# Kernel optimization log

Hardware: AMD Instinct MI355X
Metric: run time of the kernel (lower is better)

The kernel has to match this reference:

```python
import jax, jax.numpy as jnp
import numpy as np

# Coarse-to-fine lossless 3D segmentation (Seg3dLossless), batch=1, C=1.
RES = [17, 33, 65, 129]          # odd resolutions, stride (RF-1)/(R-1) is integral
RF = RES[-1]
B_MIN, B_MAX = -1.0, 1.0
BAL = 0.5                        # balance_value
N_CONFLICT_ITERS = 2             # fixed unroll of the data-dependent while-loop


def _mlp(pts, w1, b1, w2, b2, w3, b3):
    # query_func: occupancy MLP on normalized (x,y,z) points -> [N]
    h = jax.nn.relu(pts @ w1 + b1)
    h = jax.nn.relu(h @ w2 + b2)
    return jax.nn.sigmoid(h @ w3 + b3)[..., 0]


def _eval_grid(R, w1, b1, w2, b2, w3, b3):
    # batch_eval with align_corners=False: coords2D = (coord + 0.5)/RF, mapped to [B_MIN,B_MAX]
    s = (RF - 1) // (R - 1)
    c = jnp.arange(R, dtype=jnp.float32) * s                 # final-res integer coords
    p = (c + 0.5) / RF * (B_MAX - B_MIN) + B_MIN
    zz, yy, xx = jnp.meshgrid(p, p, p, indexing='ij')        # [D,H,W]
    pts = jnp.stack([xx, yy, zz], axis=-1).reshape(-1, 3)    # (x,y,z) order
    return _mlp(pts, w1, b1, w2, b2, w3, b3).reshape(R, R, R)


def _resize(x, R):
    # trilinear, align_corners=True: out index j -> in coord j*(in-1)/(out-1)
    c = jnp.linspace(0.0, x.shape[0] - 1.0, R)
    zz, yy, xx = jnp.meshgrid(c, c, c, indexing='ij')
    return jax.scipy.ndimage.map_coordinates(x, [zz, yy, xx], order=1, mode='nearest')


def _dilate(m):
    # smooth_conv3x3 (mean filter) followed by >0 == 3x3x3 binary dilation
    f = jax.lax.reduce_window(m.astype(jnp.float32), 0.0, jax.lax.max,
                              (3, 3, 3), (1, 1, 1), 'SAME')
    return f > 0.0


def setup_inputs() -> dict:
    key = jax.random.key(0)
    k1, k2, k3 = jax.random.split(key, 3)
    H = 64
    return {
        'w1': jax.random.normal(k1, (3, H), jnp.float32) * 0.8,
        'b1': jnp.zeros((H,), jnp.float32),
        'w2': jax.random.normal(k2, (H, H), jnp.float32) * (1.0 / np.sqrt(H)),
        'b2': jnp.zeros((H,), jnp.float32),
        'w3': jax.random.normal(k3, (H, 1), jnp.float32) * (1.0 / np.sqrt(H)),
        'b3': jnp.zeros((1,), jnp.float32),
    }


def reference(w1, b1, w2, b2, w3, b3):
    params = (w1, b1, w2, b2, w3, b3)
    # level 0: dense eval on the coarse grid
    occ = _eval_grid(RES[0], *params)                        # [R0,R0,R0]
    s0 = (RF - 1) // (RES[0] - 1)
    calculated = jnp.zeros((RF, RF, RF), bool).at[::s0, ::s0, ::s0].set(True)

    for R in RES[1:]:
        s = (RF - 1) // (R - 1)
        valid = _resize((occ > BAL).astype(jnp.float32), R)  # no-grad mask path
        occ_i = _resize(occ, R)                              # differentiable interp
        boundary = _dilate((valid > 0.0) & (valid < 1.0))
        calc_l = calculated[::s, ::s, ::s]
        boundary = boundary & (~calc_l)                      # skip already-evaluated voxels
        occ_true = _eval_grid(R, *params)                    # query_func at this level
        occ = jnp.where(boundary, occ_true, occ_i)           # scatter of occupancys_topk
        calc_l = calc_l | boundary
        # conflict resolution: re-query 3^3 neighbors of sign-flip voxels
        conflict = boundary & ((occ_i - BAL) * (occ_true - BAL) < 0.0)
        for _ in range(N_CONFLICT_ITERS):
            nbr = _dilate(conflict) & (~calc_l)
            occ_prev = occ
            occ = jnp.where(nbr, occ_true, occ)
            calc_l = calc_l | nbr
            conflict = nbr & ((occ_prev - BAL) * (occ_true - BAL) < 0.0)
        calculated = calculated.at[::s, ::s, ::s].set(calc_l)

    return occ[None, None]                                   # (1, 1, D, H, W)
```

## Files before the change

kernel.cpp:

```cpp
#include <hip/hip_runtime.h>

#define HH 64

static __global__ void k_set_ones(unsigned char* __restrict__ p, int n){
  int i = blockIdx.x * blockDim.x + threadIdx.x;
  if (i < n) p[i] = 1;
}

static __global__ void k_prep_w2t(const float* __restrict__ w2, float* __restrict__ w2t){
  int t = blockIdx.x * 256 + threadIdx.x;
  w2t[t] = w2[(t & 63) * HH + (t >> 6)];
}

static __global__ void k_eval_mlp(
    const float* __restrict__ w1, const float* __restrict__ b1,
    const float* __restrict__ w2t, const float* __restrict__ b2,
    const float* __restrict__ w3, const float* __restrict__ b3,
    float* __restrict__ out, int R, int s)
{
  __shared__ float sw1[3*HH];
  __shared__ float sb1[HH];
  __shared__ float sw2t[HH*HH];
  __shared__ float sb2[HH];
  __shared__ float sw3[HH];
  __shared__ float sb3s[1];
  const int t = threadIdx.x;
  {
    const float4* src4 = (const float4*)w2t;
    float4* dst4 = (float4*)sw2t;
    for (int idx = t; idx < HH*HH/4; idx += 256) dst4[idx] = src4[idx];
  }
  if (t < 3*HH) sw1[t] = w1[t];
  if (t < HH){ sb1[t] = b1[t]; sb2[t] = b2[t]; sw3[t] = w3[t]; }
  if (t == 0) sb3s[0] = b3[0];
  __syncthreads();

  const unsigned int n = (unsigned int)R * (unsigned int)R * (unsigned int)R;
  const int lane = t & 63;
  const int half = lane >> 5;
  const int ibase = half * 32;
  const unsigned int gwave = (blockIdx.x * 256u + (unsigned int)t) >> 6;
  const unsigned int pid = gwave * 32u + (unsigned int)(lane & 31);
  if (pid >= n) return;

  const unsigned int c = pid % (unsigned int)R;
  const unsigned int r = pid / (unsigned int)R;
  const unsigned int b = r % (unsigned int)R;
  const unsigned int a = r / (unsigned int)R;
  const float inv129x2 = 2.0f / 129.0f;
  const float x = ((float)(c * (unsigned int)s) + 0.5f) * inv129x2 - 1.0f;
  const float y = ((float)(b * (unsigned int)s) + 0.5f) * inv129x2 - 1.0f;
  const float z = ((float)(a * (unsigned int)s) + 0.5f) * inv129x2 - 1.0f;

  float h1[32];
  #pragma unroll
  for (int k = 0; k < 32; ++k){
    int i = ibase + k;
    float v = sb1[i];
    v = fmaf(x, sw1[i],        v);
    v = fmaf(y, sw1[HH + i],   v);
    v = fmaf(z, sw1[2*HH + i], v);
    h1[k] = fmaxf(v, 0.0f);
  }
  float o = sb3s[0];
  #pragma unroll 4
  for (int j = 0; j < HH; ++j){
    const float* wr = &sw2t[j*HH + ibase];
    float acc = 0.0f;
    #pragma unroll
    for (int k = 0; k < 32; ++k) acc = fmaf(h1[k], wr[k], acc);
    acc += __shfl_xor(acc, 32);
    o = fmaf(fmaxf(acc + sb2[j], 0.0f), sw3[j], o);
  }
  if (half == 0) out[pid] = 1.0f / (1.0f + expf(-o));
}

static __global__ void k_eval_sparse(
    const float* __restrict__ w1, const float* __restrict__ b1,
    const float* __restrict__ w2t, const float* __restrict__ b2,
    const float* __restrict__ w3, const float* __restrict__ b3,
    const int* __restrict__ idxl, const unsigned int* __restrict__ cnt,
    const float* __restrict__ occ_i,
    float* __restrict__ out, unsigned char* __restrict__ mism,
    int R, int s)
{
  const unsigned int count = *cnt;
  const unsigned int chunks = (count + 127u) >> 7;
  if (blockIdx.x >= chunks) return;
  __shared__ float sw1[3*HH];
  __shared__ float sb1[HH];
  __shared__ float sw2t[HH*HH];
  __shared__ float sb2[HH];
  __shared__ float sw3[HH];
  __shared__ float sb3s[1];
  const int t = threadIdx.x;
  {
    const float4* src4 = (const float4*)w2t;
    float4* dst4 = (float4*)sw2t;
    for (int idx = t; idx < HH*HH/4; idx += 256) dst4[idx] = src4[idx];
  }
  if (t < 3*HH) sw1[t] = w1[t];
  if (t < HH){ sb1[t] = b1[t]; sb2[t] = b2[t]; sw3[t] = w3[t]; }
  if (t == 0) sb3s[0] = b3[0];
  __syncthreads();

  const int lane = t & 63;
  const int half = lane >> 5;
  const int ibase = half * 32;
  const int wid = t >> 6;
  const float inv129x2 = 2.0f / 129.0f;

  for (unsigned int chunk = blockIdx.x; chunk < chunks; chunk += gridDim.x){
    const unsigned int slot = chunk * 128u + (unsigned int)(wid * 32 + (lane & 31));
    if (slot >= count) continue;
    const unsigned int pid = (unsigned int)idxl[slot];

    const unsigned int c = pid % (unsigned int)R;
    const unsigned int r = pid / (unsigned int)R;
    const unsigned int b = r % (unsigned int)R;
    const unsigned int a = r / (unsigned int)R;
    const float x = ((float)(c * (unsigned int)s) + 0.5f) * inv129x2 - 1.0f;
    const float y = ((float)(b * (unsigned int)s) + 0.5f) * inv129x2 - 1.0f;
    const float z = ((float)(a * (unsigned int)s) + 0.5f) * inv129x2 - 1.0f;

    float h1[32];
    #pragma unroll
    for (int k = 0; k < 32; ++k){
      int i = ibase + k;
      float v = sb1[i];
      v = fmaf(x, sw1[i],        v);
      v = fmaf(y, sw1[HH + i],   v);
      v = fmaf(z, sw1[2*HH + i], v);
      h1[k] = fmaxf(v, 0.0f);
    }
    float o = sb3s[0];
    #pragma unroll 4
    for (int j = 0; j < HH; ++j){
      const float* wr = &sw2t[j*HH + ibase];
      float acc = 0.0f;
      #pragma unroll
      for (int k = 0; k < 32; ++k) acc = fmaf(h1[k], wr[k], acc);
      acc += __shfl_xor(acc, 32);
      o = fmaf(fmaxf(acc + sb2[j], 0.0f), sw3[j], o);
    }
    if (half == 0){
      float ot = 1.0f / (1.0f + expf(-o));
      out[pid] = ot;
      mism[pid] = ((occ_i[pid] - 0.5f) * (ot - 0.5f) < 0.0f) ? (unsigned char)1 : (unsigned char)0;
    }
  }
}

static __global__ __launch_bounds__(256) void k_resize_b0(
    const float* __restrict__ prev,
    const unsigned char* __restrict__ calc_prev,
    float* __restrict__ occ_i,
    float* __restrict__ occ_out,
    unsigned char* __restrict__ bnd0,
    unsigned char* __restrict__ calc_out,
    unsigned char* __restrict__ confA,
    unsigned char* __restrict__ confB,
    unsigned char* __restrict__ upd,
    int R, int Rp)
{
  const unsigned int n = (unsigned int)R * (unsigned int)R * (unsigned int)R;
  unsigned int gid = blockIdx.x * 256u + threadIdx.x;
  if (gid >= n) return;
  int c = (int)(gid % (unsigned int)R);
  unsigned int r = gid / (unsigned int)R;
  int b = (int)(r % (unsigned int)R);
  int a = (int)(r / (unsigned int)R);
  int a0 = a >> 1, da = a & 1;
  int b0i = b >> 1, db = b & 1;
  int c0 = c >> 1, dc = c & 1;
  float sum = 0.0f;
  int cnt = 0;
  const int tot = (da + 1) * (db + 1) * (dc + 1);
  for (int dz = 0; dz <= da; ++dz)
    for (int dy = 0; dy <= db; ++dy)
      for (int dx = 0; dx <= dc; ++dx){
        float v = prev[((unsigned int)(a0 + dz) * (unsigned int)Rp + (unsigned int)(b0i + dy)) * (unsigned int)Rp + (unsigned int)(c0 + dx)];
        sum += v;
        cnt += (v > 0.5f) ? 1 : 0;
      }
  float oi = sum / (float)tot;
  occ_i[gid] = oi;
  occ_out[gid] = oi;
  bnd0[gid] = (cnt > 0 && cnt < tot) ? 1 : 0;
  calc_out[gid] = ((da | db | dc) == 0)
      ? calc_prev[((unsigned int)a0 * (unsigned int)Rp + (unsigned int)b0i) * (unsigned int)Rp + (unsigned int)c0]
      : (unsigned char)0;
  confA[gid] = 0; confB[gid] = 0; upd[gid] = 0;
}

static __global__ __launch_bounds__(256) void k_resize_boundary(
    const float* __restrict__ prev, const float* __restrict__ occ_true,
    const unsigned char* __restrict__ calc_prev,
    float* __restrict__ occ_i, float* __restrict__ occ_out,
    unsigned char* __restrict__ bnd0,
    unsigned char* __restrict__ mism, unsigned char* __restrict__ calc_out,
    int R, int Rp)
{
  const unsigned int n = (unsigned int)R * (unsigned int)R * (unsigned int)R;
  unsigned int gid = blockIdx.x * 256u + threadIdx.x;
  if (gid >= n) return;
  int c = (int)(gid % (unsigned int)R);
  unsigned int r = gid / (unsigned int)R;
  int b = (int)(r % (unsigned int)R);
  int a = (int)(r / (unsigned int)R);
  int a0 = a >> 1, da = a & 1;
  int b0i = b >> 1, db = b & 1;
  int c0 = c >> 1, dc = c & 1;
  float sum = 0.0f;
  int cnt = 0;
  const int tot = (da + 1) * (db + 1) * (dc + 1);
  for (int dz = 0; dz <= da; ++dz)
    for (int dy = 0; dy <= db; ++dy)
      for (int dx = 0; dx <= dc; ++dx){
        float v = prev[((unsigned int)(a0 + dz) * (unsigned int)Rp + (unsigned int)(b0i + dy)) * (unsigned int)Rp + (unsigned int)(c0 + dx)];
        sum += v;
        cnt += (v > 0.5f) ? 1 : 0;
      }
  float oi = sum / (float)tot;
  occ_i[gid] = oi;
  occ_out[gid] = oi;
  bnd0[gid] = (cnt > 0 && cnt < tot) ? 1 : 0;
  mism[gid] = ((oi - 0.5f) * (occ_true[gid] - 0.5f) < 0.0f) ? 1 : 0;
  calc_out[gid] = ((da | db | dc) == 0)
      ? calc_prev[((unsigned int)a0 * (unsigned int)Rp + (unsigned int)b0i) * (unsigned int)Rp + (unsigned int)c0]
      : (unsigned char)0;
}

static __global__ __launch_bounds__(256) void k_dil7x(
    const unsigned char* __restrict__ in, unsigned char* __restrict__ outp, int R)
{
  const unsigned int n = (unsigned int)R * (unsigned int)R * (unsigned int)R;
  unsigned int gid = blockIdx.x * 256u + threadIdx.x;
  if (gid >= n) return;
  int c = (int)(gid % (unsigned int)R);
  int g = (int)gid;
  int m = 0;
  #pragma unroll
  for (int d = -3; d <= 3; ++d){
    int q = c + d;
    if (q >= 0 && q < R) m |= in[g + d];
  }
  outp[gid] = (unsigned char)(m ? 1 : 0);
}

static __global__ __launch_bounds__(256) void k_dil7yz_count(
    const unsigned char* __restrict__ in, unsigned char* __restrict__ outp,
    unsigned int* __restrict__ bcnt, int R)
{
  const unsigned int n = (unsigned int)R * (unsigned int)R * (unsigned int)R;
  unsigned int gid = blockIdx.x * 256u + threadIdx.x;
  int m = 0;
  if (gid < n){
    int c = (int)(gid % (unsigned int)R);
    unsigned int r = gid / (unsigned int)R;
    int b = (int)(r % (unsigned int)R);
    int a = (int)(r / (unsigned int)R);
    int base = (int)gid;
    for (int dz = -3; dz <= 3; ++dz){
      int az = a + dz; if (az < 0 || az >= R) continue;
      for (int dy = -3; dy <= 3; ++dy){
        int by = b + dy; if (by < 0 || by >= R) continue;
        m |= in[base + dz * R * R + dy * R];
      }
    }
    outp[gid] = (unsigned char)(m ? 1 : 0);
    (void)c;
  }
  unsigned long long bm = __ballot(m != 0);
  __shared__ unsigned int wc[4];
  int wid = (int)(threadIdx.x >> 6);
  if ((threadIdx.x & 63u) == 0) wc[wid] = (unsigned int)__popcll(bm);
  __syncthreads();
  if (threadIdx.x == 0) bcnt[blockIdx.x] = wc[0] + wc[1] + wc[2] + wc[3];
}

static __global__ __launch_bounds__(1024) void k_scan(
    unsigned int* __restrict__ bcnt, unsigned int nb, unsigned int* __restrict__ total)
{
  __shared__ unsigned int part[1024];
  const unsigned int t = threadIdx.x;
  const unsigned int chunk = (nb + 1023u) / 1024u;
  const unsigned int beg = t * chunk;
  const unsigned int end = (beg + chunk < nb) ? (beg + chunk) : nb;
  unsigned int s = 0;
  for (unsigned int i = beg; i < end; ++i) s += bcnt[i];
  part[t] = s;
  __syncthreads();
  for (int offd = 1; offd < 1024; offd <<= 1){
    unsigned int v = (t >= (unsigned int)offd) ? part[t - offd] : 0u;
    __syncthreads();
    part[t] += v;
    __syncthreads();
  }
  unsigned int run = (t == 0) ? 0u : part[t - 1];
  for (unsigned int i = beg; i < end; ++i){
    unsigned int v = bcnt[i];
    bcnt[i] = run;
    run += v;
  }
  if (t == 1023) *total = part[1023];
}

static __global__ __launch_bounds__(256) void k_scatter(
    const unsigned char* __restrict__ cand, const unsigned int* __restrict__ boff,
    int* __restrict__ idxl, unsigned int n)
{
  unsigned int gid = blockIdx.x * 256u + threadIdx.x;
  bool pred = (gid < n) && (cand[gid] != 0);
  unsigned long long m = __ballot(pred);
  __shared__ unsigned int wbase[4];
  int wid = (int)(threadIdx.x >> 6);
  int lane = (int)(threadIdx.x & 63u);
  if (lane == 0) wbase[wid] = (unsigned int)__popcll(m);
  __syncthreads();
  if (threadIdx.x == 0){
    unsigned int b = boff[blockIdx.x];
    unsigned int t0 = wbase[0], t1 = wbase[1], t2 = wbase[2];
    wbase[0] = b; wbase[1] = b + t0; wbase[2] = b + t0 + t1; wbase[3] = b + t0 + t1 + t2;
  }
  __syncthreads();
  if (pred){
    int pre = __popcll(m & ((1ull << lane) - 1ull));
    idxl[wbase[wid] + (unsigned int)pre] = (int)gid;
  }
}

static __global__ __launch_bounds__(256) void k_dilate_sparse(
    const int* __restrict__ idxl, const unsigned int* __restrict__ cnt,
    const unsigned char* __restrict__ src, const unsigned char* __restrict__ mism,
    unsigned char* __restrict__ calc, unsigned char* __restrict__ conf_out,
    unsigned char* __restrict__ upd, int R, int final_step,
    const float* __restrict__ occ_true, float* __restrict__ occ_out)
{
  const unsigned int count = *cnt;
  for (unsigned int slot = blockIdx.x * 256u + threadIdx.x; slot < count;
       slot += gridDim.x * 256u){
    int gid = idxl[slot];
    int c = gid % R;
    int r = gid / R;
    int b = r % R;
    int a = r / R;
    int m = 0;
    for (int dz = -1; dz <= 1; ++dz){
      int az = a + dz; if (az < 0 || az >= R) continue;
      for (int dy = -1; dy <= 1; ++dy){
        int by = b + dy; if (by < 0 || by >= R) continue;
        for (int dx = -1; dx <= 1; ++dx){
          int cx = c + dx; if (cx < 0 || cx >= R) continue;
          m |= src[(az * R + by) * R + cx];
        }
      }
    }
    unsigned char nb = (m && !calc[gid]) ? (unsigned char)1 : (unsigned char)0;
    conf_out[gid] = (nb && mism[gid]) ? (unsigned char)1 : (unsigned char)0;
    unsigned char u = upd[gid];
    if (nb){ calc[gid] = 1; if (!u){ upd[gid] = 1; u = 1; } }
    if (final_step && u) occ_out[gid] = occ_true[gid];
  }
}

static __global__ __launch_bounds__(256) void k_dilate_step(
    const unsigned char* __restrict__ src, const unsigned char* __restrict__ mism,
    unsigned char* __restrict__ calc, unsigned char* __restrict__ conf_out,
    unsigned char* __restrict__ upd, int R, int first, int final_step,
    const float* __restrict__ occ_true, float* __restrict__ occ_out)
{
  const unsigned int n = (unsigned int)R * (unsigned int)R * (unsigned int)R;
  unsigned int gid = blockIdx.x * 256u + threadIdx.x;
  if (gid >= n) return;
  int c = (int)(gid % (unsigned int)R);
  unsigned int r = gid / (unsigned int)R;
  int b = (int)(r % (unsigned int)R);
  int a = (int)(r / (unsigned int)R);
  int m = 0;
  for (int dz = -1; dz <= 1; ++dz){
    int az = a + dz; if (az < 0 || az >= R) continue;
    for (int dy = -1; dy <= 1; ++dy){
      int by = b + dy; if (by < 0 || by >= R) continue;
      for (int dx = -1; dx <= 1; ++dx){
        int cx = c + dx; if (cx < 0 || cx >= R) continue;
        m |= src[((unsigned int)az * (unsigned int)R + (unsigned int)by) * (unsigned int)R + (unsigned int)cx];
      }
    }
  }
  unsigned char nb = (m && !calc[gid]) ? (unsigned char)1 : (unsigned char)0;
  if (nb) calc[gid] = 1;
  conf_out[gid] = (nb && mism[gid]) ? (unsigned char)1 : (unsigned char)0;
  unsigned char u;
  if (first){ u = nb; upd[gid] = nb; }
  else { u = upd[gid]; if (nb && !u){ upd[gid] = 1; u = 1; } }
  if (final_step && u) occ_out[gid] = occ_true[gid];
}

extern "C" void kernel_launch(void* const* d_in, const int* in_sizes, int n_in,
                              void* d_out, int out_size, void* d_ws, size_t ws_size,
                              hipStream_t stream)
{
  const float* w1 = (const float*)d_in[0];
  const float* b1 = (const float*)d_in[1];
  const float* w2 = (const float*)d_in[2];
  const float* b2 = (const float*)d_in[3];
  const float* w3 = (const float*)d_in[4];
  const float* b3 = (const float*)d_in[5];
  float* out = (float*)d_out;

  const int NF = 129 * 129 * 129;
  const int NP = 65 * 65 * 65;
  char* ws = (char*)d_ws;
  size_t off = 0;
  auto alloc = [&](size_t bytes) -> void* {
    void* p = (void*)(ws + off);
    off += (bytes + 255) & ~(size_t)255;
    return p;
  };
  float* f_true  = (float*)alloc((size_t)NF * 4);
  float* f_occi  = (float*)alloc((size_t)NF * 4);
  float* f_prevA = (float*)alloc((size_t)NP * 4);
  float* f_prevB = (float*)alloc((size_t)NP * 4);
  float* f_w2t   = (float*)alloc((size_t)HH * HH * 4);
  int*   i_idx   = (int*)alloc((size_t)NF * 4);
  unsigned int* u_cnt  = (unsigned int*)alloc(256);
  unsigned int* u_bcnt = (unsigned int*)alloc(8448 * 4);
  unsigned char* b_b0    = (unsigned char*)alloc(NF);
  unsigned char* b_mism  = (unsigned char*)alloc(NF);
  unsigned char* b_confA = (unsigned char*)alloc(NF);
  unsigned char* b_confB = (unsigned char*)alloc(NF);
  unsigned char* b_calcA = (unsigned char*)alloc(NF);
  unsigned char* b_calcB = (unsigned char*)alloc(NF);
  unsigned char* b_upd   = (unsigned char*)alloc(NF);
  unsigned char* b_cand  = (unsigned char*)alloc(NF);
  unsigned char* b_tmp   = (unsigned char*)alloc(NF);
  (void)ws_size;

  auto eval_blocks = [](int n){ return (n + 127) / 128; };

  k_prep_w2t<<<16, 256, 0, stream>>>(w2, f_w2t);

  {
    int R = 17, s = 8;
    int n = R * R * R;
    k_eval_mlp<<<eval_blocks(n), 256, 0, stream>>>(w1, b1, f_w2t, b2, w3, b3, f_prevA, R, s);
    k_set_ones<<<(n + 255) / 256, 256, 0, stream>>>(b_calcA, n);
  }

  int Rp = 17;
  float* prev = f_prevA;
  unsigned char* calcP = b_calcA;
  unsigned char* calcC = b_calcB;
  for (int li = 1; li <= 3; ++li){
    int R = 2 * Rp - 1;
    int s = 128 / (R - 1);
    unsigned int n = (unsigned int)R * (unsigned int)R * (unsigned int)R;
    int blocks = (int)((n + 255u) / 256u);
    float* occ_out = (li == 3) ? out : ((prev == f_prevA) ? f_prevB : f_prevA);

    if (R == 33){
      k_eval_mlp<<<eval_blocks((int)n), 256, 0, stream>>>(w1, b1, f_w2t, b2, w3, b3, f_true, R, s);
      k_resize_boundary<<<blocks, 256, 0, stream>>>(prev, f_true, calcP, f_occi, occ_out, b_b0, b_mism, calcC, R, Rp);
      k_dilate_step<<<blocks, 256, 0, stream>>>(b_b0,    b_mism, calcC, b_confA, b_upd, R, 1, 0, f_true, occ_out);
      k_dilate_step<<<blocks, 256, 0, stream>>>(b_confA, b_mism, calcC, b_confB, b_upd, R, 0, 0, f_true, occ_out);
      k_dilate_step<<<blocks, 256, 0, stream>>>(b_confB, b_mism, calcC, b_confA, b_upd, R, 0, 1, f_true, occ_out);
    } else {
      k_resize_b0<<<blocks, 256, 0, stream>>>(prev, calcP, f_occi, occ_out, b_b0, calcC,
                                              b_confA, b_confB, b_upd, R, Rp);
      k_dil7x<<<blocks, 256, 0, stream>>>(b_b0, b_tmp, R);
      k_dil7yz_count<<<blocks, 256, 0, stream>>>(b_tmp, b_cand, u_bcnt, R);
      k_scan<<<1, 1024, 0, stream>>>(u_bcnt, (unsigned int)blocks, u_cnt);
      k_scatter<<<blocks, 256, 0, stream>>>(b_cand, u_bcnt, i_idx, n);
      int egrid = eval_blocks((int)n); if (egrid > 2048) egrid = 2048;
      k_eval_sparse<<<egrid, 256, 0, stream>>>(
          w1, b1, f_w2t, b2, w3, b3, i_idx, u_cnt, f_occi, f_true, b_mism, R, s);
      int sblocks = blocks < 4096 ? blocks : 4096;
      k_dilate_sparse<<<sblocks, 256, 0, stream>>>(i_idx, u_cnt, b_b0,    b_mism, calcC, b_confA, b_upd, R, 0, f_true, occ_out);
      k_dilate_sparse<<<sblocks, 256, 0, stream>>>(i_idx, u_cnt, b_confA, b_mism, calcC, b_confB, b_upd, R, 0, f_true, occ_out);
      k_dilate_sparse<<<sblocks, 256, 0, stream>>>(i_idx, u_cnt, b_confB, b_mism, calcC, b_confA, b_upd, R, 1, f_true, occ_out);
    }

    prev = occ_out;
    unsigned char* tmpc = calcP; calcP = calcC; calcC = tmpc;
    Rp = R;
  }
  (void)in_sizes; (void)n_in; (void)out_size;
}
```

Before: 340.1 us.

## Evaluate MLP one point per thread from global weights, split y/z dilation passes

The MLP kernels drop the shared-memory weight staging and the two-lanes-per-point split with a cross-half shuffle. Each thread now evaluates a full 64-wide hidden layer for one point, reading weights from global memory, which are wave-uniform and cache-friendly. The sparse eval kernel stops using a grid-stride loop and launches one thread per candidate slot. The 7x7 y/z dilation is split into separate 7-tap y and z passes with an extra launch. The 64-float h1 array per thread raises register pressure, and global weight reads may cost more than the LDS reads they replace.

```diff
diff --git a/kernel.cpp b/kernel.cpp
--- a/kernel.cpp
+++ b/kernel.cpp
@@ -12,37 +12,42 @@
   w2t[t] = w2[(t & 63) * HH + (t >> 6)];
 }
 
-static __global__ void k_eval_mlp(
+__device__ __forceinline__ float mlp_eval(
+    const float* __restrict__ w1, const float* __restrict__ b1,
+    const float* __restrict__ w2t, const float* __restrict__ b2,
+    const float* __restrict__ w3, const float* __restrict__ b3,
+    float x, float y, float z)
+{
+  float h1[HH];
+  #pragma unroll
+  for (int i = 0; i < HH; ++i){
+    float v = b1[i];
+    v = fmaf(x, w1[i],        v);
+    v = fmaf(y, w1[HH + i],   v);
+    v = fmaf(z, w1[2*HH + i], v);
+    h1[i] = fmaxf(v, 0.0f);
+  }
+  float o = b3[0];
+  #pragma unroll 2
+  for (int j = 0; j < HH; ++j){
+    float acc = b2[j];
+    const float* wr = &w2t[j*HH];
+    #pragma unroll
+    for (int k = 0; k < HH; ++k) acc = fmaf(h1[k], wr[k], acc);
+    o = fmaf(fmaxf(acc, 0.0f), w3[j], o);
+  }
+  return 1.0f / (1.0f + expf(-o));
+}
+
+static __global__ __launch_bounds__(256, 4) void k_eval_mlp(
     const float* __restrict__ w1, const float* __restrict__ b1,
     const float* __restrict__ w2t, const float* __restrict__ b2,
     const float* __restrict__ w3, const float* __restrict__ b3,
     float* __restrict__ out, int R, int s)
 {
-  __shared__ float sw1[3*HH];
-  __shared__ float sb1[HH];
-  __shared__ float sw2t[HH*HH];
-  __shared__ float sb2[HH];
-  __shared__ float sw3[HH];
-  __shared__ float sb3s[1];
-  const int t = threadIdx.x;
-  {
-    const float4* src4 = (const float4*)w2t;
-    float4* dst4 = (float4*)sw2t;
-    for (int idx = t; idx < HH*HH/4; idx += 256) dst4[idx] = src4[idx];
-  }
-  if (t < 3*HH) sw1[t] = w1[t];
-  if (t < HH){ sb1[t] = b1[t]; sb2[t] = b2[t]; sw3[t] = w3[t]; }
-  if (t == 0) sb3s[0] = b3[0];
-  __syncthreads();
-
-  const unsigned int n = (unsigned int)R * (unsigned int)R * (unsigned int)R;
-  const int lane = t & 63;
-  const int half = lane >> 5;
-  const int ibase = half * 32;
-  const unsigned int gwave = (blockIdx.x * 256u + (unsigned int)t) >> 6;
-  const unsigned int pid = gwave * 32u + (unsigned int)(lane & 31);
+  const unsigned int n = (unsigned int)R * (unsigned int)R * (unsigned int)R;
+  unsigned int pid = blockIdx.x * 256u + threadIdx.x;
   if (pid >= n) return;
-
   const unsigned int c = pid % (unsigned int)R;
   const unsigned int r = pid / (unsigned int)R;
   const unsigned int b = r % (unsigned int)R;
@@ -51,104 +56,36 @@
   const float x = ((float)(c * (unsigned int)s) + 0.5f) * inv129x2 - 1.0f;
   const float y = ((float)(b * (unsigned int)s) + 0.5f) * inv129x2 - 1.0f;
   const float z = ((float)(a * (unsigned int)s) + 0.5f) * inv129x2 - 1.0f;
-
-  float h1[32];
-  #pragma unroll
-  for (int k = 0; k < 32; ++k){
-    int i = ibase + k;
-    float v = sb1[i];
-    v = fmaf(x, sw1[i],        v);
-    v = fmaf(y, sw1[HH + i],   v);
-    v = fmaf(z, sw1[2*HH + i], v);
-    h1[k] = fmaxf(v, 0.0f);
-  }
-  float o = sb3s[0];
-  #pragma unroll 4
-  for (int j = 0; j < HH; ++j){
-    const float* wr = &sw2t[j*HH + ibase];
-    float acc = 0.0f;
-    #pragma unroll
-    for (int k = 0; k < 32; ++k) acc = fmaf(h1[k], wr[k], acc);
-    acc += __shfl_xor(acc, 32);
-    o = fmaf(fmaxf(acc + sb2[j], 0.0f), sw3[j], o);
-  }
-  if (half == 0) out[pid] = 1.0f / (1.0f + expf(-o));
-}
-
-static __global__ void k_eval_sparse(
+  out[pid] = mlp_eval(w1, b1, w2t, b2, w3, b3, x, y, z);
+}
+
+static __global__ __launch_bounds__(256, 4) void k_eval_sparse(
     const float* __restrict__ w1, const float* __restrict__ b1,
     const float* __restrict__ w2t, const float* __restrict__ b2,
     const float* __restrict__ w3, const float* __restrict__ b3,
     const int* __restrict__ idxl, const unsigned int* __restrict__ cnt,
     const float* __restrict__ occ_i,
     float* __restrict__ out, unsigned char* __restrict__ mism,
-    int R, int s)
-{
-  const unsigned int count = *cnt;
-  const unsigned int chunks = (count + 127u) >> 7;
-  if (blockIdx.x >= chunks) return;
-  __shared__ float sw1[3*HH];
-  __shared__ float sb1[HH];
-  __shared__ float sw2t[HH*HH];
-  __shared__ float sb2[HH];
-  __shared__ float sw3[HH];
-  __shared__ float sb3s[1];
-  const int t = threadIdx.x;
-  {
-    const float4* src4 = (const float4*)w2t;
-    float4* dst4 = (float4*)sw2t;
-    for (int idx = t; idx < HH*HH/4; idx += 256) dst4[idx] = src4[idx];
-  }
-  if (t < 3*HH) sw1[t] = w1[t];
-  if (t < HH){ sb1[t] = b1[t]; sb2[t] = b2[t]; sw3[t] = w3[t]; }
-  if (t == 0) sb3s[0] = b3[0];
-  __syncthreads();
-
-  const int lane = t & 63;
-  const int half = lane >> 5;
-  const int ibase = half * 32;
-  const int wid = t >> 6;
+    int R, int s, unsigned int n)
+{
+  unsigned int count = *cnt;
+  if (count > n) count = n;
+  const unsigned int slot = blockIdx.x * 256u + threadIdx.x;
+  if (slot >= count) return;
+  const unsigned int pid = (unsigned int)idxl[slot];
+
+  const unsigned int c = pid % (unsigned int)R;
+  const unsigned int r = pid / (unsigned int)R;
+  const unsigned int b = r % (unsigned int)R;
+  const unsigned int a = r / (unsigned int)R;
   const float inv129x2 = 2.0f / 129.0f;
-
-  for (unsigned int chunk = blockIdx.x; chunk < chunks; chunk += gridDim.x){
-    const unsigned int slot = chunk * 128u + (unsigned int)(wid * 32 + (lane & 31));
-    if (slot >= count) continue;
-    const unsigned int pid = (unsigned int)idxl[slot];
-
-    const unsigned int c = pid % (unsigned int)R;
-    const unsigned int r = pid / (unsigned int)R;
-    const unsigned int b = r % (unsigned int)R;
-    const unsigned int a = r / (unsigned int)R;
-    const float x = ((float)(c * (unsigned int)s) + 0.5f) * inv129x2 - 1.0f;
-    const float y = ((float)(b * (unsigned int)s) + 0.5f) * inv129x2 - 1.0f;
-    const float z = ((float)(a * (unsigned int)s) + 0.5f) * inv129x2 - 1.0f;
-
-    float h1[32];
-    #pragma unroll
-    for (int k = 0; k < 32; ++k){
-      int i = ibase + k;
-      float v = sb1[i];
-      v = fmaf(x, sw1[i],        v);
-      v = fmaf(y, sw1[HH + i],   v);
-      v = fmaf(z, sw1[2*HH + i], v);
-      h1[k] = fmaxf(v, 0.0f);
-    }
-    float o = sb3s[0];
-    #pragma unroll 4
-    for (int j = 0; j < HH; ++j){
-      const float* wr = &sw2t[j*HH + ibase];
-      float acc = 0.0f;
-      #pragma unroll
-      for (int k = 0; k < 32; ++k) acc = fmaf(h1[k], wr[k], acc);
-      acc += __shfl_xor(acc, 32);
-      o = fmaf(fmaxf(acc + sb2[j], 0.0f), sw3[j], o);
-    }
-    if (half == 0){
-      float ot = 1.0f / (1.0f + expf(-o));
-      out[pid] = ot;
-      mism[pid] = ((occ_i[pid] - 0.5f) * (ot - 0.5f) < 0.0f) ? (unsigned char)1 : (unsigned char)0;
-    }
-  }
+  const float x = ((float)(c * (unsigned int)s) + 0.5f) * inv129x2 - 1.0f;
+  const float y = ((float)(b * (unsigned int)s) + 0.5f) * inv129x2 - 1.0f;
+  const float z = ((float)(a * (unsigned int)s) + 0.5f) * inv129x2 - 1.0f;
+
+  float ot = mlp_eval(w1, b1, w2t, b2, w3, b3, x, y, z);
+  out[pid] = ot;
+  mism[pid] = ((occ_i[pid] - 0.5f) * (ot - 0.5f) < 0.0f) ? (unsigned char)1 : (unsigned char)0;
 }
 
 static __global__ __launch_bounds__(256) void k_resize_b0(
@@ -248,7 +185,25 @@
   outp[gid] = (unsigned char)(m ? 1 : 0);
 }
 
-static __global__ __launch_bounds__(256) void k_dil7yz_count(
+static __global__ __launch_bounds__(256) void k_dil7y(
+    const unsigned char* __restrict__ in, unsigned char* __restrict__ outp, int R)
+{
+  const unsigned int n = (unsigned int)R * (unsigned int)R * (unsigned int)R;
+  unsigned int gid = blockIdx.x * 256u + threadIdx.x;
+  if (gid >= n) return;
+  unsigned int r = gid / (unsigned int)R;
+  int b = (int)(r % (unsigned int)R);
+  int g = (int)gid;
+  int m = 0;
+  #pragma unroll
+  for (int d = -3; d <= 3; ++d){
+    int q = b + d;
+    if (q >= 0 && q < R) m |= in[g + d * R];
+  }
+  outp[gid] = (unsigned char)(m ? 1 : 0);
+}
+
+static __global__ __launch_bounds__(256) void k_dil7z_count(
     const unsigned char* __restrict__ in, unsigned char* __restrict__ outp,
     unsigned int* __restrict__ bcnt, int R)
 {
@@ -256,20 +211,15 @@
   unsigned int gid = blockIdx.x * 256u + threadIdx.x;
   int m = 0;
   if (gid < n){
-    int c = (int)(gid % (unsigned int)R);
-    unsigned int r = gid / (unsigned int)R;
-    int b = (int)(r % (unsigned int)R);
-    int a = (int)(r / (unsigned int)R);
-    int base = (int)gid;
-    for (int dz = -3; dz <= 3; ++dz){
-      int az = a + dz; if (az < 0 || az >= R) continue;
-      for (int dy = -3; dy <= 3; ++dy){
-        int by = b + dy; if (by < 0 || by >= R) continue;
-        m |= in[base + dz * R * R + dy * R];
-      }
+    int a = (int)(gid / ((unsigned int)R * (unsigned int)R));
+    int g = (int)gid;
+    int RR = R * R;
+    #pragma unroll
+    for (int d = -3; d <= 3; ++d){
+      int q = a + d;
+      if (q >= 0 && q < R) m |= in[g + d * RR];
     }
     outp[gid] = (unsigned char)(m ? 1 : 0);
-    (void)c;
   }
   unsigned long long bm = __ballot(m != 0);
   __shared__ unsigned int wc[4];
@@ -335,9 +285,11 @@
     const unsigned char* __restrict__ src, const unsigned char* __restrict__ mism,
     unsigned char* __restrict__ calc, unsigned char* __restrict__ conf_out,
     unsigned char* __restrict__ upd, int R, int final_step,
-    const float* __restrict__ occ_true, float* __restrict__ occ_out)
-{
-  const unsigned int count = *cnt;
+    const float* __restrict__ occ_true, float* __restrict__ occ_out,
+    unsigned int n)
+{
+  unsigned int count = *cnt;
+  if (count > n) count = n;
   for (unsigned int slot = blockIdx.x * 256u + threadIdx.x; slot < count;
        slot += gridDim.x * 256u){
     int gid = idxl[slot];
@@ -437,15 +389,14 @@
   unsigned char* b_tmp   = (unsigned char*)alloc(NF);
   (void)ws_size;
 
-  auto eval_blocks = [](int n){ return (n + 127) / 128; };
-
   k_prep_w2t<<<16, 256, 0, stream>>>(w2, f_w2t);
 
   {
     int R = 17, s = 8;
     int n = R * R * R;
-    k_eval_mlp<<<eval_blocks(n), 256, 0, stream>>>(w1, b1, f_w2t, b2, w3, b3, f_prevA, R, s);
-    k_set_ones<<<(n + 255) / 256, 256, 0, stream>>>(b_calcA, n);
+    int blocks = (n + 255) / 256;
+    k_eval_mlp<<<blocks, 256, 0, stream>>>(w1, b1, f_w2t, b2, w3, b3, f_prevA, R, s);
+    k_set_ones<<<blocks, 256, 0, stream>>>(b_calcA, n);
   }
 
   int Rp = 17;
@@ -460,7 +411,7 @@
     float* occ_out = (li == 3) ? out : ((prev == f_prevA) ? f_prevB : f_prevA);
 
     if (R == 33){
-      k_eval_mlp<<<eval_blocks((int)n), 256, 0, stream>>>(w1, b1, f_w2t, b2, w3, b3, f_true, R, s);
+      k_eval_mlp<<<blocks, 256, 0, stream>>>(w1, b1, f_w2t, b2, w3, b3, f_true, R, s);
       k_resize_boundary<<<blocks, 256, 0, stream>>>(prev, f_true, calcP, f_occi, occ_out, b_b0, b_mism, calcC, R, Rp);
       k_dilate_step<<<blocks, 256, 0, stream>>>(b_b0,    b_mism, calcC, b_confA, b_upd, R, 1, 0, f_true, occ_out);
       k_dilate_step<<<blocks, 256, 0, stream>>>(b_confA, b_mism, calcC, b_confB, b_upd, R, 0, 0, f_true, occ_out);
@@ -468,17 +419,17 @@
     } else {
       k_resize_b0<<<blocks, 256, 0, stream>>>(prev, calcP, f_occi, occ_out, b_b0, calcC,
                                               b_confA, b_confB, b_upd, R, Rp);
-      k_dil7x<<<blocks, 256, 0, stream>>>(b_b0, b_tmp, R);
-      k_dil7yz_count<<<blocks, 256, 0, stream>>>(b_tmp, b_cand, u_bcnt, R);
+      k_dil7x<<<blocks, 256, 0, stream>>>(b_b0,  b_tmp,  R);
+      k_dil7y<<<blocks, 256, 0, stream>>>(b_tmp, b_cand, R);
+      k_dil7z_count<<<blocks, 256, 0, stream>>>(b_cand, b_tmp, u_bcnt, R);
       k_scan<<<1, 1024, 0, stream>>>(u_bcnt, (unsigned int)blocks, u_cnt);
-      k_scatter<<<blocks, 256, 0, stream>>>(b_cand, u_bcnt, i_idx, n);
-      int egrid = eval_blocks((int)n); if (egrid > 2048) egrid = 2048;
-      k_eval_sparse<<<egrid, 256, 0, stream>>>(
-          w1, b1, f_w2t, b2, w3, b3, i_idx, u_cnt, f_occi, f_true, b_mism, R, s);
+      k_scatter<<<blocks, 256, 0, stream>>>(b_tmp, u_bcnt, i_idx, n);
+      k_eval_sparse<<<blocks, 256, 0, stream>>>(
+          w1, b1, f_w2t, b2, w3, b3, i_idx, u_cnt, f_occi, f_true, b_mism, R, s, n);
       int sblocks = blocks < 4096 ? blocks : 4096;
-      k_dilate_sparse<<<sblocks, 256, 0, stream>>>(i_idx, u_cnt, b_b0,    b_mism, calcC, b_confA, b_upd, R, 0, f_true, occ_out);
-      k_dilate_sparse<<<sblocks, 256, 0, stream>>>(i_idx, u_cnt, b_confA, b_mism, calcC, b_confB, b_upd, R, 0, f_true, occ_out);
-      k_dilate_sparse<<<sblocks, 256, 0, stream>>>(i_idx, u_cnt, b_confB, b_mism, calcC, b_confA, b_upd, R, 1, f_true, occ_out);
+      k_dilate_sparse<<<sblocks, 256, 0, stream>>>(i_idx, u_cnt, b_b0,    b_mism, calcC, b_confA, b_upd, R, 0, f_true, occ_out, n);
+      k_dilate_sparse<<<sblocks, 256, 0, stream>>>(i_idx, u_cnt, b_confA, b_mism, calcC, b_confB, b_upd, R, 0, f_true, occ_out, n);
+      k_dilate_sparse<<<sblocks, 256, 0, stream>>>(i_idx, u_cnt, b_confB, b_mism, calcC, b_confA, b_upd, R, 1, f_true, occ_out, n);
     }
 
     prev = occ_out;
```

After: 353.6 us. 1.04x slower.
